# Kernel optimization log

Hardware: AMD Instinct MI355X
Metric: run time of the kernel (lower is better)

The kernel has to match this reference:

```python
import jax, jax.numpy as jnp
import numpy as np

N_EMB = 1024
E_DIM = 256


def setup_inputs() -> dict:
    key = jax.random.key(0)
    k1, k2 = jax.random.split(key)
    z = jax.random.normal(k1, (32, E_DIM, 64, 64), dtype=jnp.float32)
    # torch init: uniform_(-1/e_dim, 1/e_dim)
    emb = jax.random.uniform(k2, (N_EMB, E_DIM), dtype=jnp.float32,
                             minval=-1.0 / E_DIM, maxval=1.0 / E_DIM)
    return {"z": z, "emb": emb}


def reference(z, emb):
    # z: [bs, c, h, w] -> [bs, h, w, c] -> [N, e_dim]
    zp = jnp.transpose(z, (0, 2, 3, 1))
    zf = zp.reshape(-1, emb.shape[1])
    # squared euclidean distance via ||z||^2 + ||e||^2 - 2 z.e
    z_sq = jnp.sum(zf * zf, axis=1, keepdims=True)          # [N, 1]
    e_sq = jnp.sum(emb * emb, axis=1)                        # [n_emb]
    e_z = jnp.matmul(zf, emb.T)                              # [N, n_emb]
    dist = z_sq + e_sq - 2.0 * e_z
    idx = jnp.argmin(dist, axis=1)                           # [N] int
    z_q = emb[idx].reshape(zp.shape)                         # [bs, h, w, c]
    z_q = jnp.transpose(z_q, (0, 3, 1, 2))                   # [bs, c, h, w]
    return z_q, idx
```

## Files before the change

### kernel.cpp

```cpp
#include <hip/hip_runtime.h>
#include <float.h>

#define NEMB 1024
#define EDIM 256
#define BM   64
#define HW   4096
#define NB   16
#define NT   1024
#define NW   (NT / 64)
#define ZQ_ELEMS 33554432

template <typename F>
__device__ __forceinline__ float np_sumsq_256(F get) {
#pragma clang fp contract(off)
    float blk[2];
#pragma unroll
    for (int h = 0; h < 2; ++h) {
        const int base = h * 128;
        float r[8];
#pragma unroll
        for (int j = 0; j < 8; ++j) {
            float v = get(base + j);
            r[j] = v * v;
        }
        for (int i = 8; i < 128; i += 8) {
#pragma unroll
            for (int j = 0; j < 8; ++j) {
                float v = get(base + i + j);
                float p = v * v;
                r[j] = r[j] + p;
            }
        }
        blk[h] = ((r[0] + r[1]) + (r[2] + r[3])) + ((r[4] + r[5]) + (r[6] + r[7]));
    }
    return blk[0] + blk[1];
}

__global__ __launch_bounds__(256) void esq_kernel(const float* __restrict__ emb,
                                                  float* __restrict__ esq) {
    int n = blockIdx.x * 256 + threadIdx.x;
    const float* e = emb + (size_t)n * EDIM;
    esq[n] = np_sumsq_256([&](int k) { return e[k]; });
}

__global__ __launch_bounds__(NT, 8) void vq_kernel(const float* __restrict__ z,
                                                   const float* __restrict__ emb,
                                                   const float* __restrict__ esq,
                                                   float* __restrict__ out) {
    __shared__ float zl[BM * EDIM];

    const int t   = threadIdx.x;
    const int blk = blockIdx.x;
    const int b   = blk >> 6;
    const int hw0 = (blk & 63) * BM;
    const float* zb = z + (size_t)b * EDIM * HW;

#pragma unroll
    for (int pass = 0; pass < 4; ++pass) {
        int f4 = pass * NT + t;
        int r4 = (f4 & 15) * 4;
        int k  = f4 >> 4;
        float4 v = *(const float4*)(zb + (size_t)k * HW + hw0 + r4);
        int w = (k >> 1) * 128 + 2 * r4 + (k & 1);
        zl[w + 0] = v.x;
        zl[w + 2] = v.y;
        zl[w + 4] = v.z;
        zl[w + 6] = v.w;
    }
    __syncthreads();

    const int r = t & 63;
    const float* zr = zl + 2 * r;
    const float zsq = np_sumsq_256([&](int k) { return zr[(k >> 1) * 128 + (k & 1)]; });

    const int q = __builtin_amdgcn_readfirstlane(t >> 6);

    float best = FLT_MAX;
    int   bidx = 0;
#pragma unroll 1
    for (int g = 0; g < 4; ++g) {
        const int n0 = q * 64 + g * NB;
        float acc[NB];
#pragma unroll
        for (int j = 0; j < NB; ++j) acc[j] = 0.f;

        float2 zk[4], zk2[4];
#pragma unroll
        for (int u = 0; u < 4; ++u) zk[u] = *(const float2*)(zr + u * 128);
        for (int k = 0; k < EDIM; k += 16) {
#pragma unroll
            for (int u = 0; u < 4; ++u)
                zk2[u] = *(const float2*)(zr + ((k + 8) >> 1) * 128 + u * 128);
#pragma unroll
            for (int jh = 0; jh < 2; ++jh) {
                const float* eb = emb + (size_t)(n0 + jh * 8) * EDIM + k;
#pragma unroll
                for (int u = 0; u < 8; ++u) {
                    const float zv = (u & 1) ? zk[u >> 1].y : zk[u >> 1].x;
#pragma unroll
                    for (int j2 = 0; j2 < 8; ++j2)
                        acc[jh * 8 + j2] = fmaf(zv, eb[(size_t)j2 * EDIM + u],
                                                acc[jh * 8 + j2]);
                }
            }
            if (k + 16 < EDIM) {
#pragma unroll
                for (int u = 0; u < 4; ++u)
                    zk[u] = *(const float2*)(zr + ((k + 16) >> 1) * 128 + u * 128);
            }
#pragma unroll
            for (int jh = 0; jh < 2; ++jh) {
                const float* eb = emb + (size_t)(n0 + jh * 8) * EDIM + k + 8;
#pragma unroll
                for (int u = 0; u < 8; ++u) {
                    const float zv = (u & 1) ? zk2[u >> 1].y : zk2[u >> 1].x;
#pragma unroll
                    for (int j2 = 0; j2 < 8; ++j2)
                        acc[jh * 8 + j2] = fmaf(zv, eb[(size_t)j2 * EDIM + u],
                                                acc[jh * 8 + j2]);
                }
            }
        }
#pragma unroll
        for (int j = 0; j < NB; ++j) {
            float t1 = zsq + esq[n0 + j];
            float d  = fmaf(-2.f, acc[j], t1);
            if (d < best) { best = d; bidx = n0 + j; }
        }
    }

    __syncthreads();
    float* rv   = zl;
    int*   ri   = (int*)(zl + NT);
    int*   ifin = (int*)(zl + 2 * NT);
    rv[t] = best;
    ri[t] = bidx;
    __syncthreads();
    if (t < 64) {
        float bv = rv[t];
        int   bi = ri[t];
#pragma unroll
        for (int w = 1; w < NW; ++w) {
            float v = rv[t + 64 * w];
            int   i = ri[t + 64 * w];
            if (v < bv) { bv = v; bi = i; }
        }
        ifin[t] = bi;
        out[(size_t)ZQ_ELEMS + (size_t)blk * BM + t] = (float)bi;
    }
    __syncthreads();

    float* zq = out + (size_t)b * EDIM * HW;
#pragma unroll
    for (int pass = 0; pass < 4; ++pass) {
        int f4 = pass * NT + t;
        int r4 = (f4 & 15) * 4;
        int c  = f4 >> 4;
        float4 v;
        v.x = emb[(size_t)ifin[r4 + 0] * EDIM + c];
        v.y = emb[(size_t)ifin[r4 + 1] * EDIM + c];
        v.z = emb[(size_t)ifin[r4 + 2] * EDIM + c];
        v.w = emb[(size_t)ifin[r4 + 3] * EDIM + c];
        *(float4*)(zq + (size_t)c * HW + hw0 + r4) = v;
    }
}

extern "C" void kernel_launch(void* const* d_in, const int* in_sizes, int n_in,
                              void* d_out, int out_size, void* d_ws, size_t ws_size,
                              hipStream_t stream) {
    const float* z   = (const float*)d_in[0];
    const float* emb = (const float*)d_in[1];
    float* out = (float*)d_out;
    float* esq = (float*)d_ws;

    esq_kernel<<<NEMB / 256, 256, 0, stream>>>(emb, esq);
    vq_kernel<<<131072 / BM, NT, 0, stream>>>(z, emb, esq, out);
}
```

Measured before the change: 1.253 ms.

## Accumulate all 64 codebook rows per wave in one pass over the embedding dimension

Replaces the four sequential groups of 16 codes, each of which re-read the whole 256-dim z row from LDS, with a single pass keeping 64 accumulators in registers. z chunks of 16 values are double-buffered from LDS and each chunk is reused across all 64 codes. The emb loads are wave-uniform, so they can be scalar loads. Launch bounds drop to 4 blocks per SM to allow the larger register footprint, which reduces occupancy and raises spill risk.

```diff
diff --git a/kernel.cpp b/kernel.cpp
--- a/kernel.cpp
+++ b/kernel.cpp
@@ -5,7 +5,6 @@
 #define EDIM 256
 #define BM   64
 #define HW   4096
-#define NB   16
 #define NT   1024
 #define NW   (NT / 64)
 #define ZQ_ELEMS 33554432
@@ -43,7 +42,7 @@
     esq[n] = np_sumsq_256([&](int k) { return e[k]; });
 }
 
-__global__ __launch_bounds__(NT, 8) void vq_kernel(const float* __restrict__ z,
+__global__ __launch_bounds__(NT, 4) void vq_kernel(const float* __restrict__ z,
                                                    const float* __restrict__ emb,
                                                    const float* __restrict__ esq,
                                                    float* __restrict__ out) {
@@ -53,14 +52,14 @@
     const int blk = blockIdx.x;
     const int b   = blk >> 6;
     const int hw0 = (blk & 63) * BM;
-    const float* zb = z + (size_t)b * EDIM * HW;
+    const float* zbase = z + (size_t)b * EDIM * HW;
 
 #pragma unroll
     for (int pass = 0; pass < 4; ++pass) {
         int f4 = pass * NT + t;
         int r4 = (f4 & 15) * 4;
         int k  = f4 >> 4;
-        float4 v = *(const float4*)(zb + (size_t)k * HW + hw0 + r4);
+        float4 v = *(const float4*)(zbase + (size_t)k * HW + hw0 + r4);
         int w = (k >> 1) * 128 + 2 * r4 + (k & 1);
         zl[w + 0] = v.x;
         zl[w + 2] = v.y;
@@ -73,60 +72,51 @@
     const float* zr = zl + 2 * r;
     const float zsq = np_sumsq_256([&](int k) { return zr[(k >> 1) * 128 + (k & 1)]; });
 
-    const int q = __builtin_amdgcn_readfirstlane(t >> 6);
+    const int q  = __builtin_amdgcn_readfirstlane(t >> 6);
+    const int n0 = q * 64;
+
+    float acc[64];
+#pragma unroll
+    for (int n = 0; n < 64; ++n) acc[n] = 0.f;
+
+    float2 zA[8], zB[8];
+    auto ldz = [&](float2* dst, int kbase) {
+        const int m0 = kbase >> 1;
+#pragma unroll
+        for (int u = 0; u < 8; ++u)
+            dst[u] = *(const float2*)(zr + (m0 + u) * 128);
+    };
+    auto fmablk = [&](const float2* zc, int kbase) {
+#pragma unroll
+        for (int n = 0; n < 64; ++n) {
+            const float* er = emb + (size_t)(n0 + n) * EDIM + kbase;
+            float a = acc[n];
+#pragma unroll
+            for (int u = 0; u < 8; ++u) {
+                a = fmaf(zc[u].x, er[2 * u + 0], a);
+                a = fmaf(zc[u].y, er[2 * u + 1], a);
+            }
+            acc[n] = a;
+        }
+    };
+
+    ldz(zA, 0);
+#pragma unroll 1
+    for (int c = 0; c < 8; ++c) {
+        const int k0 = c * 32;
+        ldz(zB, k0 + 16);
+        fmablk(zA, k0);
+        if (c < 7) ldz(zA, k0 + 32);
+        fmablk(zB, k0 + 16);
+    }
 
     float best = FLT_MAX;
     int   bidx = 0;
-#pragma unroll 1
-    for (int g = 0; g < 4; ++g) {
-        const int n0 = q * 64 + g * NB;
-        float acc[NB];
 #pragma unroll
-        for (int j = 0; j < NB; ++j) acc[j] = 0.f;
-
-        float2 zk[4], zk2[4];
-#pragma unroll
-        for (int u = 0; u < 4; ++u) zk[u] = *(const float2*)(zr + u * 128);
-        for (int k = 0; k < EDIM; k += 16) {
-#pragma unroll
-            for (int u = 0; u < 4; ++u)
-                zk2[u] = *(const float2*)(zr + ((k + 8) >> 1) * 128 + u * 128);
-#pragma unroll
-            for (int jh = 0; jh < 2; ++jh) {
-                const float* eb = emb + (size_t)(n0 + jh * 8) * EDIM + k;
-#pragma unroll
-                for (int u = 0; u < 8; ++u) {
-                    const float zv = (u & 1) ? zk[u >> 1].y : zk[u >> 1].x;
-#pragma unroll
-                    for (int j2 = 0; j2 < 8; ++j2)
-                        acc[jh * 8 + j2] = fmaf(zv, eb[(size_t)j2 * EDIM + u],
-                                                acc[jh * 8 + j2]);
-                }
-            }
-            if (k + 16 < EDIM) {
-#pragma unroll
-                for (int u = 0; u < 4; ++u)
-                    zk[u] = *(const float2*)(zr + ((k + 16) >> 1) * 128 + u * 128);
-            }
-#pragma unroll
-            for (int jh = 0; jh < 2; ++jh) {
-                const float* eb = emb + (size_t)(n0 + jh * 8) * EDIM + k + 8;
-#pragma unroll
-                for (int u = 0; u < 8; ++u) {
-                    const float zv = (u & 1) ? zk2[u >> 1].y : zk2[u >> 1].x;
-#pragma unroll
-                    for (int j2 = 0; j2 < 8; ++j2)
-                        acc[jh * 8 + j2] = fmaf(zv, eb[(size_t)j2 * EDIM + u],
-                                                acc[jh * 8 + j2]);
-                }
-            }
-        }
-#pragma unroll
-        for (int j = 0; j < NB; ++j) {
-            float t1 = zsq + esq[n0 + j];
-            float d  = fmaf(-2.f, acc[j], t1);
-            if (d < best) { best = d; bidx = n0 + j; }
-        }
+    for (int n = 0; n < 64; ++n) {
+        float t1 = zsq + esq[n0 + n];
+        float d  = fmaf(-2.f, acc[n], t1);
+        if (d < best) { best = d; bidx = n0 + n; }
     }
 
     __syncthreads();
```

New measurement: 4.717 ms. 3.76x slower.
